# Performance work log

Hardware: AMD Instinct MI355X
Metric: run time of the kernel (lower is better)

The kernel has to match this reference:

```python
import jax, jax.numpy as jnp
import numpy as np

TEMPERATURE = 0.3
BASE_TEMPERATURE = 0.07
EPS = 1e-08


def setup_inputs() -> dict:
    key = jax.random.key(0)
    k1, k2 = jax.random.split(key)
    bsz, n_views, f_dim = 4096, 2, 128
    features = jax.random.normal(k1, (bsz, n_views, f_dim), dtype=jnp.float32)
    # L2-normalize as is standard for contrastive features (keeps logits well-scaled)
    features = features / jnp.linalg.norm(features, axis=-1, keepdims=True)
    labels = jax.random.randint(k2, (bsz,), 0, 2, dtype=jnp.int64)
    return {"features": features, "labels": labels}


def reference(features, labels):
    # features: [B, V, D], labels: [B]
    B, V, D = features.shape
    N = B * V

    # mask[i,j] = 1 if labels[i] == labels[j]
    mask = (labels[:, None] == labels[None, :]).astype(jnp.float32)  # [B, B]

    # torch.cat(torch.unbind(features, dim=1), dim=0): view-major stacking -> [V*B, D]
    contrast_feature = features.transpose(1, 0, 2).reshape(N, D)
    anchor_feature = contrast_feature  # contrast_mode == 'all'

    logits = jnp.matmul(anchor_feature, contrast_feature.T) / TEMPERATURE  # [N, N]
    logits = logits - jax.lax.stop_gradient(jnp.max(logits, axis=1, keepdims=True))

    mask = jnp.tile(mask, (V, V))  # [N, N]
    logits_mask = 1.0 - jnp.eye(N, dtype=jnp.float32)  # mask out self-contrast
    mask = mask * logits_mask

    exp_logits = jnp.exp(logits) * logits_mask
    log_prob = logits - jnp.log(jnp.sum(exp_logits, axis=1, keepdims=True) + EPS)

    mean_log_prob_pos = jnp.sum(mask * log_prob, axis=1) / (jnp.sum(mask, axis=1) + EPS)
    loss = -(TEMPERATURE / BASE_TEMPERATURE) * mean_log_prob_pos  # [N]
    return jnp.mean(loss.reshape(V, B))
```

## Files before the change

kernel.cpp:

```cpp
#include <hip/hip_runtime.h>
#include <hip/hip_bf16.h>

constexpr int B_SZ  = 4096;
constexpr int N_SZ  = 8192;
constexpr int CHUNK = 512;
constexpr int TILE  = 64;
constexpr int NT    = CHUNK / TILE;
constexpr int NCH   = N_SZ / CHUNK;
constexpr int BROWS = 128;

typedef __attribute__((ext_vector_type(8))) __bf16 bf16x8;
typedef __attribute__((ext_vector_type(4))) float f32x4;

#define SQRT_CSC  2.1929404f
#define NEG_RATIO (-(0.3f / 0.07f))

__device__ __forceinline__ unsigned short f2bf(float f) {
    unsigned u = __float_as_uint(f);
    u += 0x7FFFu + ((u >> 16) & 1u);
    return (unsigned short)(u >> 16);
}

__device__ __forceinline__ void gl_lds16(const unsigned short* g, unsigned short* l) {
    __builtin_amdgcn_global_load_lds(
        (const __attribute__((address_space(1))) unsigned int*)g,
        (__attribute__((address_space(3))) unsigned int*)l, 16, 0, 0);
}

__global__ __launch_bounds__(256) void prep_kernel(const float* __restrict__ feat,
                                                   unsigned short* __restrict__ A,
                                                   float* __restrict__ out) {
    const int tid = threadIdx.x;
    if (blockIdx.x == 0 && tid == 0) out[0] = 0.f;
    int t = blockIdx.x * 256 + tid;
    int n = t >> 5;
    int q = (t & 31) << 2;
    int b = n & (B_SZ - 1);
    int v = n >> 12;
    const float4 f = *reinterpret_cast<const float4*>(feat + (((size_t)b * 2 + v) << 7) + q);
    ushort4 o;
    o.x = f2bf(f.x * SQRT_CSC); o.y = f2bf(f.y * SQRT_CSC);
    o.z = f2bf(f.z * SQRT_CSC); o.w = f2bf(f.w * SQRT_CSC);
    *reinterpret_cast<ushort4*>(A + (((size_t)n) << 7) + q) = o;
}

__global__ __launch_bounds__(256) void msum_kernel(const float* __restrict__ feat,
                                                   const int* __restrict__ labels,
                                                   float* __restrict__ mpart) {
    __shared__ float sm[2][256];
    const int tid = threadIdx.x;
    const int v = tid >> 7, d = tid & 127;
    const int b0 = blockIdx.x * 16;
    float a0 = 0.f, a1 = 0.f;
#pragma unroll
    for (int it = 0; it < 16; ++it) {
        const int b = b0 + it;
        const float x = feat[(((size_t)b * 2 + v) << 7) + d];
        if (labels[b]) a1 += x; else a0 += x;
    }
    sm[0][tid] = a0; sm[1][tid] = a1;
    __syncthreads();
    if (tid < 128)
        mpart[(size_t)tid * 256 + blockIdx.x] = sm[0][tid] + sm[0][tid + 128];
    else
        mpart[(size_t)tid * 256 + blockIdx.x] = sm[1][tid - 128] + sm[1][tid];
}

__global__ __launch_bounds__(256) void mreduce_kernel(const float* __restrict__ mpart,
                                                      const int* __restrict__ labels,
                                                      float* __restrict__ mvec,
                                                      int* __restrict__ cnt) {
    __shared__ int redi[4];
    const int tid = threadIdx.x;
    const float* p = mpart + (size_t)tid * 256;
    float s = 0.f;
#pragma unroll 8
    for (int k = 0; k < 256; k += 4) {
        const float4 x = *reinterpret_cast<const float4*>(p + k);
        s += x.x + x.y + x.z + x.w;
    }
    mvec[tid] = s;
    int c = 0;
    for (int i = tid; i < B_SZ; i += 256) c += labels[i];
#pragma unroll
    for (int m = 1; m < 64; m <<= 1) c += __shfl_xor(c, m);
    if ((tid & 63) == 0) redi[tid >> 6] = c;
    __syncthreads();
    if (tid == 0) *cnt = redi[0] + redi[1] + redi[2] + redi[3];
}

__global__ __launch_bounds__(256, 2) void gram_kernel(const unsigned short* __restrict__ A,
                                                      float* __restrict__ S_part) {
    __shared__ __align__(16) unsigned short tb[2][TILE * 128];

    const int tid  = threadIdx.x;
    const int wave = tid >> 6;
    const int lane = tid & 63;
    const int grp  = lane >> 4;
    const int lc   = lane & 15;
    const int row0 = blockIdx.x * BROWS + wave * 32;
    const int col0 = blockIdx.y * CHUNK;

    bf16x8 a[2][4];
#pragma unroll
    for (int rt = 0; rt < 2; ++rt) {
        const unsigned short* ap = A + ((size_t)(row0 + 16 * rt + lc) << 7) + grp * 8;
#pragma unroll
        for (int g = 0; g < 4; ++g)
            a[rt][g] = *reinterpret_cast<const bf16x8*>(ap + g * 32);
    }

    float s_acc[2][4] = {{0,0,0,0},{0,0,0,0}};

    auto stage = [&](int buf, int tt) {
        const unsigned short* gbase = A + ((size_t)(col0 + tt * TILE) << 7);
#pragma unroll
        for (int k = 0; k < 4; ++k) {
            const int s = tid + 256 * k;
            const int r = s >> 4, c = s & 15;
            const int src = (r << 4) + (c ^ (r & 7));
            gl_lds16(gbase + src * 8, &tb[buf][s * 8]);
        }
    };

    stage(0, 0);
    __syncthreads();

#pragma clang loop unroll(disable)
    for (int t = 0; t < NT; ++t) {
        const int cur = t & 1;
        if (t + 1 < NT) stage(cur ^ 1, t + 1);

#pragma unroll
        for (int ct = 0; ct < 4; ++ct) {
            const int tc = 16 * ct + lc;
            const unsigned short* rowp = &tb[cur][tc * 128];
            bf16x8 bfr[4];
#pragma unroll
            for (int g = 0; g < 4; ++g)
                bfr[g] = *reinterpret_cast<const bf16x8*>(rowp + (((4 * g + grp) ^ (tc & 7)) << 3));

            f32x4 acc0 = {0,0,0,0}, acc1 = {0,0,0,0};
#pragma unroll
            for (int g = 0; g < 4; ++g) {
                acc0 = __builtin_amdgcn_mfma_f32_16x16x32_bf16(a[0][g], bfr[g], acc0, 0, 0, 0);
                acc1 = __builtin_amdgcn_mfma_f32_16x16x32_bf16(a[1][g], bfr[g], acc1, 0, 0, 0);
            }

            const int colT = col0 + t * TILE + 16 * ct;
#pragma unroll
            for (int rt = 0; rt < 2; ++rt) {
                const f32x4 acc = rt ? acc1 : acc0;
                if (colT == row0 + 16 * rt) {
#pragma unroll
                    for (int r = 0; r < 4; ++r)
                        s_acc[rt][r] += (lc == 4 * grp + r) ? 0.f : __builtin_exp2f(acc[r]);
                } else {
#pragma unroll
                    for (int r = 0; r < 4; ++r)
                        s_acc[rt][r] += __builtin_exp2f(acc[r]);
                }
            }
        }
        __syncthreads();
    }

#pragma unroll
    for (int m = 1; m < 16; m <<= 1)
#pragma unroll
        for (int rt = 0; rt < 2; ++rt)
#pragma unroll
            for (int r = 0; r < 4; ++r)
                s_acc[rt][r] += __shfl_xor(s_acc[rt][r], m);

    if (lc == 0) {
        const size_t base = (size_t)blockIdx.y * N_SZ;
#pragma unroll
        for (int rt = 0; rt < 2; ++rt)
#pragma unroll
            for (int r = 0; r < 4; ++r)
                S_part[base + row0 + 16 * rt + 4 * grp + r] = s_acc[rt][r];
    }
}

__global__ __launch_bounds__(256) void final_kernel(const float* __restrict__ S_part,
                                                    const float* __restrict__ feat,
                                                    const int* __restrict__ labels,
                                                    const float* __restrict__ mvec,
                                                    const int* __restrict__ cnt,
                                                    float* __restrict__ out) {
    __shared__ float red[4];
    const int tid = threadIdx.x;
    const int i = blockIdx.x * 256 + tid;

    float S = 0.f;
#pragma unroll
    for (int k = 0; k < NCH; ++k) S += S_part[(size_t)k * N_SZ + i];

    const int b = i & (B_SZ - 1), v = i >> 12;
    const int lab = labels[b];
    const float* fr = feat + (((size_t)b * 2 + v) << 7);
    const float* mv = mvec + (lab ? 128 : 0);
    float dot = 0.f;
#pragma unroll 8
    for (int d = 0; d < 128; d += 4) {
        const float4 x = *reinterpret_cast<const float4*>(fr + d);
        const float4 y = *reinterpret_cast<const float4*>(mv + d);
        dot += x.x * y.x + x.y * y.y + x.z * y.z + x.w * y.w;
    }

    const int c1 = *cnt;
    const int cs = lab ? c1 : (B_SZ - c1);
    const float n = (float)(2 * cs - 1);
    float term = ((dot - 1.0f) * (1.0f / 0.3f) - n * logf(S + 1e-8f)) / (n + 1e-8f);

#pragma unroll
    for (int m = 1; m < 64; m <<= 1) term += __shfl_xor(term, m);
    if ((tid & 63) == 0) red[tid >> 6] = term;
    __syncthreads();
    if (tid == 0)
        atomicAdd(out, (red[0] + red[1] + red[2] + red[3]) * (NEG_RATIO / (float)N_SZ));
}

extern "C" void kernel_launch(void* const* d_in, const int* in_sizes, int n_in,
                              void* d_out, int out_size, void* d_ws, size_t ws_size,
                              hipStream_t stream) {
    const float* feat = (const float*)d_in[0];
    const int* labels = (const int*)d_in[1];
    float* out = (float*)d_out;

    char* ws = (char*)d_ws;
    unsigned short* A = (unsigned short*)ws;
    float* S_part = (float*)(ws + (size_t)2 * 1024 * 1024);
    float* mpart  = (float*)(ws + (size_t)2 * 1024 * 1024 + 512 * 1024);
    float* mvec   = (float*)(ws + (size_t)2 * 1024 * 1024 + 768 * 1024);
    int*   cnt    = (int*)(ws + (size_t)2 * 1024 * 1024 + 769 * 1024);

    prep_kernel<<<dim3(1024), dim3(256), 0, stream>>>(feat, A, out);
    msum_kernel<<<dim3(256), dim3(256), 0, stream>>>(feat, labels, mpart);
    mreduce_kernel<<<dim3(1), dim3(256), 0, stream>>>(mpart, labels, mvec, cnt);
    gram_kernel<<<dim3(N_SZ / BROWS, NCH), dim3(256), 0, stream>>>(A, S_part);
    final_kernel<<<dim3(N_SZ / 256), dim3(256), 0, stream>>>(S_part, feat, labels, mvec, cnt, out);
}
```

Measured before the change: 55.93 us.

## Fuse class-sum into prep, reduce in final kernel, and loosen gram pipeline barriers

The per-class feature sums are now built inside the prep kernel with LDS atomics, and their reduction plus the label count move into the final kernel. This drops two separate launches (msum and mreduce). The gram kernel loop now waits on explicit vmcnt/lgkmcnt counters with raw barriers instead of __syncthreads, so the next tile's loads can overlap compute, and it precomputes the swizzled LDS offsets. In exchange, every final block re-reduces a 256x1024 partial array, which is redundant work. The gram loop also issues one extra wrapped-around stage load on its last iteration.

```diff
diff --git a/kernel.cpp b/kernel.cpp
--- a/kernel.cpp
+++ b/kernel.cpp
@@ -8,6 +8,7 @@
 constexpr int NT    = CHUNK / TILE;
 constexpr int NCH   = N_SZ / CHUNK;
 constexpr int BROWS = 128;
+constexpr int MP_W  = 1024;
 
 typedef __attribute__((ext_vector_type(8))) __bf16 bf16x8;
 typedef __attribute__((ext_vector_type(4))) float f32x4;
@@ -28,65 +29,32 @@
 }
 
 __global__ __launch_bounds__(256) void prep_kernel(const float* __restrict__ feat,
+                                                   const int* __restrict__ labels,
                                                    unsigned short* __restrict__ A,
+                                                   float* __restrict__ mpart,
                                                    float* __restrict__ out) {
+    __shared__ float cls[256];
     const int tid = threadIdx.x;
-    if (blockIdx.x == 0 && tid == 0) out[0] = 0.f;
-    int t = blockIdx.x * 256 + tid;
-    int n = t >> 5;
-    int q = (t & 31) << 2;
-    int b = n & (B_SZ - 1);
-    int v = n >> 12;
+    cls[tid] = 0.f;
+    __syncthreads();
+
+    const int t = blockIdx.x * 256 + tid;
+    const int n = t >> 5;
+    const int q = (t & 31) << 2;
+    const int b = n & (B_SZ - 1);
+    const int v = n >> 12;
     const float4 f = *reinterpret_cast<const float4*>(feat + (((size_t)b * 2 + v) << 7) + q);
     ushort4 o;
     o.x = f2bf(f.x * SQRT_CSC); o.y = f2bf(f.y * SQRT_CSC);
     o.z = f2bf(f.z * SQRT_CSC); o.w = f2bf(f.w * SQRT_CSC);
     *reinterpret_cast<ushort4*>(A + (((size_t)n) << 7) + q) = o;
-}
-
-__global__ __launch_bounds__(256) void msum_kernel(const float* __restrict__ feat,
-                                                   const int* __restrict__ labels,
-                                                   float* __restrict__ mpart) {
-    __shared__ float sm[2][256];
-    const int tid = threadIdx.x;
-    const int v = tid >> 7, d = tid & 127;
-    const int b0 = blockIdx.x * 16;
-    float a0 = 0.f, a1 = 0.f;
-#pragma unroll
-    for (int it = 0; it < 16; ++it) {
-        const int b = b0 + it;
-        const float x = feat[(((size_t)b * 2 + v) << 7) + d];
-        if (labels[b]) a1 += x; else a0 += x;
-    }
-    sm[0][tid] = a0; sm[1][tid] = a1;
-    __syncthreads();
-    if (tid < 128)
-        mpart[(size_t)tid * 256 + blockIdx.x] = sm[0][tid] + sm[0][tid + 128];
-    else
-        mpart[(size_t)tid * 256 + blockIdx.x] = sm[1][tid - 128] + sm[1][tid];
-}
-
-__global__ __launch_bounds__(256) void mreduce_kernel(const float* __restrict__ mpart,
-                                                      const int* __restrict__ labels,
-                                                      float* __restrict__ mvec,
-                                                      int* __restrict__ cnt) {
-    __shared__ int redi[4];
-    const int tid = threadIdx.x;
-    const float* p = mpart + (size_t)tid * 256;
-    float s = 0.f;
-#pragma unroll 8
-    for (int k = 0; k < 256; k += 4) {
-        const float4 x = *reinterpret_cast<const float4*>(p + k);
-        s += x.x + x.y + x.z + x.w;
-    }
-    mvec[tid] = s;
-    int c = 0;
-    for (int i = tid; i < B_SZ; i += 256) c += labels[i];
-#pragma unroll
-    for (int m = 1; m < 64; m <<= 1) c += __shfl_xor(c, m);
-    if ((tid & 63) == 0) redi[tid >> 6] = c;
-    __syncthreads();
-    if (tid == 0) *cnt = redi[0] + redi[1] + redi[2] + redi[3];
+
+    float* c = &cls[(labels[b] ? 128 : 0) + q];
+    atomicAdd(c + 0, f.x); atomicAdd(c + 1, f.y);
+    atomicAdd(c + 2, f.z); atomicAdd(c + 3, f.w);
+    __syncthreads();
+    mpart[(size_t)tid * MP_W + blockIdx.x] = cls[tid];
+    if (blockIdx.x == 0 && tid == 0) out[0] = 0.f;
 }
 
 __global__ __launch_bounds__(256, 2) void gram_kernel(const unsigned short* __restrict__ A,
@@ -110,6 +78,11 @@
             a[rt][g] = *reinterpret_cast<const bf16x8*>(ap + g * 32);
     }
 
+    int off[4];
+#pragma unroll
+    for (int g = 0; g < 4; ++g)
+        off[g] = lc * 128 + (((4 * g + grp) ^ (lc & 7)) << 3);
+
     float s_acc[2][4] = {{0,0,0,0},{0,0,0,0}};
 
     auto stage = [&](int buf, int tt) {
@@ -124,21 +97,21 @@
     };
 
     stage(0, 0);
-    __syncthreads();
+    int cur = 0;
 
 #pragma clang loop unroll(disable)
     for (int t = 0; t < NT; ++t) {
-        const int cur = t & 1;
-        if (t + 1 < NT) stage(cur ^ 1, t + 1);
-
+        stage(cur ^ 1, (t + 1) & (NT - 1));
+        asm volatile("s_waitcnt vmcnt(4)" ::: "memory");
+        __builtin_amdgcn_s_barrier();
+
+        const unsigned short* bp = &tb[cur][0];
 #pragma unroll
         for (int ct = 0; ct < 4; ++ct) {
-            const int tc = 16 * ct + lc;
-            const unsigned short* rowp = &tb[cur][tc * 128];
             bf16x8 bfr[4];
 #pragma unroll
             for (int g = 0; g < 4; ++g)
-                bfr[g] = *reinterpret_cast<const bf16x8*>(rowp + (((4 * g + grp) ^ (tc & 7)) << 3));
+                bfr[g] = *reinterpret_cast<const bf16x8*>(bp + ct * 2048 + off[g]);
 
             f32x4 acc0 = {0,0,0,0}, acc1 = {0,0,0,0};
 #pragma unroll
@@ -162,7 +135,10 @@
                 }
             }
         }
-        __syncthreads();
+
+        asm volatile("s_waitcnt lgkmcnt(0)" ::: "memory");
+        __builtin_amdgcn_s_barrier();
+        cur ^= 1;
     }
 
 #pragma unroll
@@ -186,13 +162,33 @@
 __global__ __launch_bounds__(256) void final_kernel(const float* __restrict__ S_part,
                                                     const float* __restrict__ feat,
                                                     const int* __restrict__ labels,
-                                                    const float* __restrict__ mvec,
-                                                    const int* __restrict__ cnt,
+                                                    const float* __restrict__ mpart,
                                                     float* __restrict__ out) {
+    __shared__ float mv[256];
     __shared__ float red[4];
+    __shared__ int   redi[4];
     const int tid = threadIdx.x;
+
+    {
+        const float* p = mpart + (size_t)tid * MP_W;
+        float s = 0.f;
+#pragma unroll 4
+        for (int k = 0; k < MP_W; k += 4) {
+            const float4 x = *reinterpret_cast<const float4*>(p + k);
+            s += x.x + x.y + x.z + x.w;
+        }
+        mv[tid] = s;
+    }
+
+    int c = 0;
+    for (int i = tid; i < B_SZ; i += 256) c += labels[i];
+#pragma unroll
+    for (int m = 1; m < 64; m <<= 1) c += __shfl_xor(c, m);
+    if ((tid & 63) == 0) redi[tid >> 6] = c;
+    __syncthreads();
+    const int c1 = redi[0] + redi[1] + redi[2] + redi[3];
+
     const int i = blockIdx.x * 256 + tid;
-
     float S = 0.f;
 #pragma unroll
     for (int k = 0; k < NCH; ++k) S += S_part[(size_t)k * N_SZ + i];
@@ -200,16 +196,14 @@
     const int b = i & (B_SZ - 1), v = i >> 12;
     const int lab = labels[b];
     const float* fr = feat + (((size_t)b * 2 + v) << 7);
-    const float* mv = mvec + (lab ? 128 : 0);
+    const float* mvp = &mv[lab ? 128 : 0];
     float dot = 0.f;
 #pragma unroll 8
     for (int d = 0; d < 128; d += 4) {
         const float4 x = *reinterpret_cast<const float4*>(fr + d);
-        const float4 y = *reinterpret_cast<const float4*>(mv + d);
-        dot += x.x * y.x + x.y * y.y + x.z * y.z + x.w * y.w;
-    }
-
-    const int c1 = *cnt;
+        dot += x.x * mvp[d] + x.y * mvp[d + 1] + x.z * mvp[d + 2] + x.w * mvp[d + 3];
+    }
+
     const int cs = lab ? c1 : (B_SZ - c1);
     const float n = (float)(2 * cs - 1);
     float term = ((dot - 1.0f) * (1.0f / 0.3f) - n * logf(S + 1e-8f)) / (n + 1e-8f);
@@ -233,12 +227,8 @@
     unsigned short* A = (unsigned short*)ws;
     float* S_part = (float*)(ws + (size_t)2 * 1024 * 1024);
     float* mpart  = (float*)(ws + (size_t)2 * 1024 * 1024 + 512 * 1024);
-    float* mvec   = (float*)(ws + (size_t)2 * 1024 * 1024 + 768 * 1024);
-    int*   cnt    = (int*)(ws + (size_t)2 * 1024 * 1024 + 769 * 1024);
-
-    prep_kernel<<<dim3(1024), dim3(256), 0, stream>>>(feat, A, out);
-    msum_kernel<<<dim3(256), dim3(256), 0, stream>>>(feat, labels, mpart);
-    mreduce_kernel<<<dim3(1), dim3(256), 0, stream>>>(mpart, labels, mvec, cnt);
+
+    prep_kernel<<<dim3(1024), dim3(256), 0, stream>>>(feat, labels, A, mpart, out);
     gram_kernel<<<dim3(N_SZ / BROWS, NCH), dim3(256), 0, stream>>>(A, S_part);
-    final_kernel<<<dim3(N_SZ / 256), dim3(256), 0, stream>>>(S_part, feat, labels, mvec, cnt, out);
-}
+    final_kernel<<<dim3(N_SZ / 256), dim3(256), 0, stream>>>(S_part, feat, labels, mpart, out);
+}
```

New measurement: 79.69 us. +42.5%, slower.
